# Kernel optimization log

Measured on AMD Instinct MI355X. Metric: run time of the kernel, lower is better.

Reference implementation:

```python
import jax, jax.numpy as jnp
import numpy as np

N, E = 50000, 400000
IN, HID, HEADS, OUT, EDIM = 128, 16, 8, 128, 32


def _lin(key, fan_in, fan_out, bias=True):
    k1, k2 = jax.random.split(key)
    s = 1.0 / np.sqrt(fan_in)
    W = jax.random.uniform(k1, (fan_in, fan_out), jnp.float32, -s, s)
    if bias:
        b = jax.random.uniform(k2, (fan_out,), jnp.float32, -s, s)
        return W, b
    return W


def setup_inputs() -> dict:
    key = jax.random.key(0)
    ks = jax.random.split(key, 16)
    x = jax.random.normal(ks[0], (N, IN), jnp.float32)
    edge_index = jax.random.randint(ks[1], (2, E), 0, N, jnp.int64)
    edge_feats = jax.random.normal(ks[2], (E, EDIM), jnp.float32)
    H1 = HEADS * HID  # 128
    Wq1, bq1 = _lin(ks[3], IN, H1)
    Wk1, bk1 = _lin(ks[4], IN, H1)
    Wv1, bv1 = _lin(ks[5], IN, H1)
    We1 = _lin(ks[6], EDIM, H1, bias=False)
    Ws1, bs1 = _lin(ks[7], IN, H1)
    Wq2, bq2 = _lin(ks[8], H1, OUT)
    Wk2, bk2 = _lin(ks[9], H1, OUT)
    Wv2, bv2 = _lin(ks[10], H1, OUT)
    We2 = _lin(ks[11], EDIM, OUT, bias=False)
    Ws2, bs2 = _lin(ks[12], H1, OUT)
    return dict(x=x, edge_index=edge_index, edge_feats=edge_feats,
                Wq1=Wq1, bq1=bq1, Wk1=Wk1, bk1=bk1, Wv1=Wv1, bv1=bv1, We1=We1, Ws1=Ws1, bs1=bs1,
                Wq2=Wq2, bq2=bq2, Wk2=Wk2, bk2=bk2, Wv2=Wv2, bv2=bv2, We2=We2, Ws2=Ws2, bs2=bs2)


def transformer_conv(x, src, dst, e, Wq, bq, Wk, bk, Wv, bv, We, Ws, bs, heads, ch, concat):
    # PyG TransformerConv: project at nodes, gather to edges.
    n = x.shape[0]
    q = (x @ Wq + bq).reshape(n, heads, ch)[dst]          # [E,H,C]
    k = (x @ Wk + bk).reshape(n, heads, ch)[src]
    v = (x @ Wv + bv).reshape(n, heads, ch)[src]
    ee = (e @ We).reshape(-1, heads, ch)                   # edge conditioning
    k = k + ee
    v = v + ee
    alpha = (q * k).sum(-1) / jnp.sqrt(jnp.asarray(ch, x.dtype))  # [E,H]
    # per-destination segment softmax
    m = jax.ops.segment_max(alpha, dst, num_segments=n)
    m = jnp.where(jnp.isfinite(m), m, 0.0)
    ea = jnp.exp(alpha - m[dst])
    denom = jax.ops.segment_sum(ea, dst, num_segments=n)
    attn = ea / jnp.maximum(denom[dst], 1e-16)
    out = jax.ops.segment_sum(attn[:, :, None] * v, dst, num_segments=n)  # [N,H,C]
    out = out.reshape(n, heads * ch) if concat else out.mean(axis=1)
    return out + x @ Ws + bs  # root_weight skip


def reference(x, edge_index, edge_feats,
              Wq1, bq1, Wk1, bk1, Wv1, bv1, We1, Ws1, bs1,
              Wq2, bq2, Wk2, bk2, Wv2, bv2, We2, Ws2, bs2):
    src, dst = edge_index[0], edge_index[1]
    h = jax.nn.relu(transformer_conv(x, src, dst, edge_feats,
                                     Wq1, bq1, Wk1, bk1, Wv1, bv1, We1, Ws1, bs1,
                                     HEADS, HID, True))
    # dropout p=0.0 (eval) -> identity
    out = jax.nn.relu(transformer_conv(h, src, dst, edge_feats,
                                       Wq2, bq2, Wk2, bk2, Wv2, bv2, We2, Ws2, bs2,
                                       1, OUT, False))
    return out
```

## Files before the change

### kernel.cpp

```cpp
#include <hip/hip_runtime.h>


using u16 = unsigned short;
using u32 = unsigned int;

#define NODES 50000
#define EDGES 400000
#define NB196 196

typedef __attribute__((ext_vector_type(8))) short bf16x8;
typedef __attribute__((ext_vector_type(4))) float f32x4;

__device__ __forceinline__ float bflo(u32 u) { return __uint_as_float(u << 16); }
__device__ __forceinline__ float bfhi(u32 u) { return __uint_as_float(u & 0xffff0000u); }
__device__ __forceinline__ u16 f2bf(float f) {
    u32 u = __float_as_uint(f);
    u += 0x7fffu + ((u >> 16) & 1u);
    return (u16)(u >> 16);
}
__device__ __forceinline__ u32 pack2(float a, float b) {
    return (u32)f2bf(a) | ((u32)f2bf(b) << 16);
}

template <int CTRL>
__device__ __forceinline__ float dpp_addf(float x) {
    int y = __builtin_amdgcn_update_dpp(0, __float_as_int(x), CTRL, 0xF, 0xF, true);
    return x + __int_as_float(y);
}
template <int GRP>
__device__ __forceinline__ float grp_sum(float p, int lane) {
    p = dpp_addf<0xB1>(p);
    p = dpp_addf<0x4E>(p);
    p = dpp_addf<0x141>(p);
    if (GRP == 64) {
        p = dpp_addf<0x140>(p);
        p += __int_as_float(__builtin_amdgcn_ds_swizzle(__float_as_int(p), 0x401F));
        p += __int_as_float(__builtin_amdgcn_ds_bpermute((lane ^ 32) << 2,
                                                         __float_as_int(p)));
    }
    return p;
}

__global__ __launch_bounds__(256) void fill_sentinel(float* __restrict__ out, int n, float val) {
    int i = blockIdx.x * 256 + threadIdx.x;
    if (i < n) out[i] = val;
}

__global__ __launch_bounds__(64) void detect_fmt(const u32* __restrict__ xw,
                                                 const int* __restrict__ eraw,
                                                 int* __restrict__ flags) {
    int lane = threadIdx.x;
    u32 e = (xw[lane] >> 7) & 0xffu;
    unsigned long long sane = __ballot(e >= 90u && e <= 141u);
    unsigned long long zodd = __ballot(eraw[1 + 2 * lane] == 0);
    if (lane == 0) {
        flags[0] = (sane == ~0ull) ? 0 : 1;
        flags[1] = (zodd == ~0ull) ? 1 : 0;
    }
}

struct TPtrs {
    const void* src[10];
    u16*        dst[10];
    int         K[10];
};

__global__ __launch_bounds__(256) void transpose_w(TPtrs P, const int* __restrict__ fmt) {
    int m = blockIdx.x;
    int f = *fmt;
    int K = P.K[m];
    int quarter = (K * 128) >> 2;
    u16* d = P.dst[m];
    int base = blockIdx.y * quarter;
    const float* sf = (const float*)P.src[m];
    const u16*   sb = (const u16*)P.src[m];
    for (int idx = base + threadIdx.x; idx < base + quarter; idx += 256) {
        int k = idx >> 7, n = idx & 127;
        d[n * K + k] = f ? f2bf(sf[idx]) : sb[idx];
    }
}

__global__ __launch_bounds__(256) void count_deg(const int* __restrict__ raw,
                                                 const int* __restrict__ flags,
                                                 int* __restrict__ deg, int E) {
    int e = blockIdx.x * 256 + threadIdx.x;
    if (e < E) {
        int f = flags[1];
        int d = f ? raw[2 * (E + e)] : raw[E + e];
        if ((unsigned)d < (unsigned)NODES) atomicAdd(&deg[d], 1);
    }
}

__device__ __forceinline__ int block_scan256(int v) {
    __shared__ int ws[4];
    int t = threadIdx.x, lane = t & 63, w = t >> 6;
    int x = v;
#pragma unroll
    for (int off = 1; off < 64; off <<= 1) {
        int y = __shfl_up(x, off, 64);
        if (lane >= off) x += y;
    }
    if (lane == 63) ws[w] = x;
    __syncthreads();
#pragma unroll
    for (int j = 0; j < 3; ++j)
        if (j < w) x += ws[j];
    return x;
}

__global__ __launch_bounds__(256) void scan_a(const int* __restrict__ deg,
                                              int* __restrict__ bsum, int n) {
    int i = blockIdx.x * 256 + threadIdx.x;
    int v = (i < n) ? deg[i] : 0;
    int incl = block_scan256(v);
    if (threadIdx.x == 255) bsum[blockIdx.x] = incl;
}

__global__ __launch_bounds__(256) void scan_b(int* __restrict__ bsum, int nb) {
    int t = threadIdx.x;
    int v = (t < nb) ? bsum[t] : 0;
    int incl = block_scan256(v);
    if (t < nb) bsum[t] = incl - v;
}

__global__ __launch_bounds__(256) void scan_c(const int* __restrict__ deg,
                                              const int* __restrict__ bsum,
                                              int* __restrict__ row_ptr,
                                              int* __restrict__ cursor, int n) {
    int b = blockIdx.x;
    int i = b * 256 + threadIdx.x;
    int v = (i < n) ? deg[i] : 0;
    int incl = block_scan256(v) + bsum[b];
    if (i < n) {
        row_ptr[i + 1] = incl;
        cursor[i] = incl - v;
    }
    if (i == 0) row_ptr[0] = 0;
}

__global__ __launch_bounds__(256) void fill_csr(const int* __restrict__ raw,
                                                const int* __restrict__ flags,
                                                int* __restrict__ cursor,
                                                int2* __restrict__ se, int E) {
    int e = blockIdx.x * 256 + threadIdx.x;
    if (e < E) {
        int f = flags[1];
        int d = f ? raw[2 * (E + e)] : raw[E + e];
        int s = f ? raw[2 * e] : raw[e];
        if ((unsigned)d < (unsigned)NODES && (unsigned)s < (unsigned)NODES) {
            int pos = atomicAdd(&cursor[d], 1);
            if ((unsigned)pos < (unsigned)E) se[pos] = make_int2(s, e);
        }
    }
}

__global__ __launch_bounds__(256) void gemm128(
    const void* __restrict__ A, const int* __restrict__ flags, int a_raw,
    const u16* __restrict__ Wt0, const u16* __restrict__ Wt1,
    const u16* __restrict__ Wt2, const u16* __restrict__ Wt3,
    const void* __restrict__ b0, const void* __restrict__ b1,
    const void* __restrict__ b2, const void* __restrict__ b3,
    u16* __restrict__ O0, u16* __restrict__ O1,
    u16* __restrict__ O2, u16* __restrict__ O3,
    int M) {
    constexpr int K = 128;
    constexpr int PAD = K + 8;
    constexpr int KV = K / 8;
    __shared__ u16 Asl[64 * PAD];
    __shared__ u16 Bsl[128 * PAD];

    int f = flags[0];
    const u16* Wt; const void* bias; u16* O;
    switch (blockIdx.y) {
        case 0: Wt = Wt0; bias = b0; O = O0; break;
        case 1: Wt = Wt1; bias = b1; O = O1; break;
        case 2: Wt = Wt2; bias = b2; O = O2; break;
        default: Wt = Wt3; bias = b3; O = O3; break;
    }
    int m0 = blockIdx.x * 64;

    if (a_raw && f) {
        const float* Af = (const float*)A;
        for (int idx = threadIdx.x; idx < 64 * KV; idx += 256) {
            int r = idx / KV, cv = idx % KV;
            int gr = m0 + r;
            uint4 val = make_uint4(0, 0, 0, 0);
            if (gr < M) {
                const float* p = Af + (size_t)gr * K + cv * 8;
                float4 lo = *reinterpret_cast<const float4*>(p);
                float4 hi = *reinterpret_cast<const float4*>(p + 4);
                val = make_uint4(pack2(lo.x, lo.y), pack2(lo.z, lo.w),
                                 pack2(hi.x, hi.y), pack2(hi.z, hi.w));
            }
            *reinterpret_cast<uint4*>(&Asl[r * PAD + cv * 8]) = val;
        }
    } else {
        const u16* Ab = (const u16*)A;
        for (int idx = threadIdx.x; idx < 64 * KV; idx += 256) {
            int r = idx / KV, cv = idx % KV;
            int gr = m0 + r;
            uint4 val = make_uint4(0, 0, 0, 0);
            if (gr < M) val = *reinterpret_cast<const uint4*>(Ab + (size_t)gr * K + cv * 8);
            *reinterpret_cast<uint4*>(&Asl[r * PAD + cv * 8]) = val;
        }
    }
    for (int idx = threadIdx.x; idx < 128 * KV; idx += 256) {
        int r = idx / KV, cv = idx % KV;
        *reinterpret_cast<uint4*>(&Bsl[r * PAD + cv * 8]) =
            *reinterpret_cast<const uint4*>(Wt + r * K + cv * 8);
    }
    __syncthreads();

    int lane = threadIdx.x & 63, wv = threadIdx.x >> 6;
    int l15 = lane & 15;
    int kq = (lane >> 4) * 8;
    f32x4 acc[8] = {};
#pragma unroll
    for (int k0 = 0; k0 < K; k0 += 32) {
        bf16x8 af = *reinterpret_cast<const bf16x8*>(&Asl[(wv * 16 + l15) * PAD + k0 + kq]);
#pragma unroll
        for (int nt = 0; nt < 8; ++nt) {
            bf16x8 bfv = *reinterpret_cast<const bf16x8*>(&Bsl[(nt * 16 + l15) * PAD + k0 + kq]);
            acc[nt] = __builtin_amdgcn_mfma_f32_16x16x32_bf16(af, bfv, acc[nt], 0, 0, 0);
        }
    }

    int rbase = m0 + wv * 16 + (lane >> 4) * 4;
#pragma unroll
    for (int nt = 0; nt < 8; ++nt) {
        int col = nt * 16 + l15;
        float bb = 0.f;
        if (bias) bb = f ? ((const float*)bias)[col] : bflo((u32)((const u16*)bias)[col]);
#pragma unroll
        for (int r = 0; r < 4; ++r) {
            int m = rbase + r;
            if (m < M) O[(size_t)m * 128 + col] = f2bf(acc[nt][r] + bb);
        }
    }
}

__global__ __launch_bounds__(256) void gemm_ee(
    const int2* __restrict__ se, const void* __restrict__ EF,
    const u16* __restrict__ WtE1 , const u16* __restrict__ WtE2,
    const int* __restrict__ flags,
    u16* __restrict__ EE1, u16* __restrict__ EE2, int Etot) {
    constexpr int PAD = 40;
    __shared__ u16 Asl[64 * PAD];
    __shared__ u16 Bsl[2][128 * PAD];
    int p0 = blockIdx.x * 64;
    int f = flags[0];
    bool dual = (EE2 != nullptr);

    {
        int r = threadIdx.x >> 2, seg = threadIdx.x & 3;
        int p = p0 + r;
        int e = (p < Etot) ? se[p].y : 0;
        uint4 val;
        if (f) {
            const float* src = (const float*)EF + (size_t)e * 32 + seg * 8;
            float4 lo = *reinterpret_cast<const float4*>(src);
            float4 hi = *reinterpret_cast<const float4*>(src + 4);
            val = make_uint4(pack2(lo.x, lo.y), pack2(lo.z, lo.w),
                             pack2(hi.x, hi.y), pack2(hi.z, hi.w));
        } else {
            val = *reinterpret_cast<const uint4*>((const u16*)EF + (size_t)e * 32 + seg * 8);
        }
        *reinterpret_cast<uint4*>(&Asl[r * PAD + seg * 8]) = val;
    }
    for (int idx = threadIdx.x; idx < 128 * 4; idx += 256) {
        int r = idx >> 2, seg = idx & 3;
        *reinterpret_cast<uint4*>(&Bsl[0][r * PAD + seg * 8]) =
            *reinterpret_cast<const uint4*>(WtE1 + r * 32 + seg * 8);
    }
    if (dual) {
        for (int idx = threadIdx.x; idx < 128 * 4; idx += 256) {
            int r = idx >> 2, seg = idx & 3;
            *reinterpret_cast<uint4*>(&Bsl[1][r * PAD + seg * 8]) =
                *reinterpret_cast<const uint4*>(WtE2 + r * 32 + seg * 8);
        }
    }
    __syncthreads();

    int lane = threadIdx.x & 63, wv = threadIdx.x >> 6;
    int l15 = lane & 15;
    int kq = (lane >> 4) * 8;
    int rbase = p0 + wv * 16 + (lane >> 4) * 4;
    bf16x8 af = *reinterpret_cast<const bf16x8*>(&Asl[(wv * 16 + l15) * PAD + kq]);

    {
        f32x4 acc[8] = {};
#pragma unroll
        for (int nt = 0; nt < 8; ++nt) {
            bf16x8 bfv = *reinterpret_cast<const bf16x8*>(&Bsl[0][(nt * 16 + l15) * PAD + kq]);
            acc[nt] = __builtin_amdgcn_mfma_f32_16x16x32_bf16(af, bfv, acc[nt], 0, 0, 0);
        }
#pragma unroll
        for (int nt = 0; nt < 8; ++nt) {
            int col = nt * 16 + l15;
#pragma unroll
            for (int r = 0; r < 4; ++r) {
                int p = rbase + r;
                if (p < Etot) EE1[(size_t)p * 128 + col] = f2bf(acc[nt][r]);
            }
        }
    }
    if (dual) {
        f32x4 acc[8] = {};
#pragma unroll
        for (int nt = 0; nt < 8; ++nt) {
            bf16x8 bfv = *reinterpret_cast<const bf16x8*>(&Bsl[1][(nt * 16 + l15) * PAD + kq]);
            acc[nt] = __builtin_amdgcn_mfma_f32_16x16x32_bf16(af, bfv, acc[nt], 0, 0, 0);
        }
#pragma unroll
        for (int nt = 0; nt < 8; ++nt) {
            int col = nt * 16 + l15;
#pragma unroll
            for (int r = 0; r < 4; ++r) {
                int p = rbase + r;
                if (p < Etot) EE2[(size_t)p * 128 + col] = f2bf(acc[nt][r]);
            }
        }
    }
}

template <int HEADS, int F32OUT, int MAT>
__global__ __launch_bounds__(256) void attn_kernel(
    const int* __restrict__ row_ptr, const int2* __restrict__ se,
    const int* __restrict__ flags,
    const u16* __restrict__ Q, const u16* __restrict__ Kn,
    const u16* __restrict__ Vn, const u16* __restrict__ EE,
    const void* __restrict__ EF, const void* __restrict__ We,
    const u16* __restrict__ SK, void* __restrict__ OUT, int nn) {
    int wv = threadIdx.x >> 6, lane = threadIdx.x & 63;
    int node = blockIdx.x * 4 + wv;
    if (node >= nn) return;
    int c0 = lane * 2;
    int f = flags[0];

    u32 qb = *reinterpret_cast<const u32*>(Q + (size_t)node * 128 + c0);
    float q0 = bflo(qb), q1 = bfhi(qb);

    int beg = row_ptr[node], end = row_ptr[node + 1];
    const float scale = (HEADS == 8) ? 0.25f : 0.08838834764831845f;
    constexpr int GRP = (HEADS == 8) ? 8 : 64;

    float l_run = 0.f, a0 = 0.f, a1 = 0.f;

    auto edge_step = [&](u32 kbv, u32 vbv, u32 ebv) {
        float e0 = bflo(ebv), e1 = bfhi(ebv);
        float k0 = bflo(kbv) + e0, k1 = bfhi(kbv) + e1;
        float p = q0 * k0 + q1 * k1;
        p = grp_sum<GRP>(p, lane);
        float w = __expf(p * scale);
        l_run += w;
        a0 = fmaf(w, bflo(vbv) + e0, a0);
        a1 = fmaf(w, bfhi(vbv) + e1, a1);
    };

    if (MAT) {
        int i = beg;
        for (; i + 8 <= end; i += 8) {
            int sA[8];
#pragma unroll
            for (int j = 0; j < 8; ++j) sA[j] = se[i + j].x;
            u32 kb[8], vb[8], eb[8];
#pragma unroll
            for (int j = 0; j < 8; ++j) {
                kb[j] = *reinterpret_cast<const u32*>(Kn + (size_t)sA[j] * 128 + c0);
                vb[j] = *reinterpret_cast<const u32*>(Vn + (size_t)sA[j] * 128 + c0);
                eb[j] = *reinterpret_cast<const u32*>(EE + (size_t)(i + j) * 128 + c0);
            }
#pragma unroll
            for (int j = 0; j < 8; ++j) edge_step(kb[j], vb[j], eb[j]);
        }
        for (; i < end; ++i) {
            int s = se[i].x;
            u32 kbv = *reinterpret_cast<const u32*>(Kn + (size_t)s * 128 + c0);
            u32 vbv = *reinterpret_cast<const u32*>(Vn + (size_t)s * 128 + c0);
            u32 ebv = *reinterpret_cast<const u32*>(EE + (size_t)i * 128 + c0);
            edge_step(kbv, vbv, ebv);
        }
    } else {
        float wf0[32], wf1[32];
        if (f) {
            const float* Wef = (const float*)We;
#pragma unroll
            for (int d = 0; d < 32; ++d) {
                float2 w2 = *reinterpret_cast<const float2*>(Wef + d * 128 + c0);
                wf0[d] = w2.x; wf1[d] = w2.y;
            }
        } else {
            const u16* Web = (const u16*)We;
#pragma unroll
            for (int d = 0; d < 32; ++d) {
                u32 w = *reinterpret_cast<const u32*>(Web + d * 128 + c0);
                wf0[d] = bflo(w); wf1[d] = bfhi(w);
            }
        }
        for (int i = beg; i < end; ++i) {
            int2 p2 = se[i];
            int s = p2.x, e = p2.y;
            u32 kbv = *reinterpret_cast<const u32*>(Kn + (size_t)s * 128 + c0);
            u32 vbv = *reinterpret_cast<const u32*>(Vn + (size_t)s * 128 + c0);
            float efv[32];
            if (f) {
                const float* eff = (const float*)EF + (size_t)e * 32;
#pragma unroll
                for (int t = 0; t < 8; ++t) {
                    float4 q4 = *reinterpret_cast<const float4*>(eff + t * 4);
                    efv[4 * t] = q4.x; efv[4 * t + 1] = q4.y;
                    efv[4 * t + 2] = q4.z; efv[4 * t + 3] = q4.w;
                }
            } else {
                const uint4* efp = reinterpret_cast<const uint4*>((const u16*)EF + (size_t)e * 32);
                uint4 efa = efp[0], efb2 = efp[1], efc = efp[2], efd = efp[3];
                u32 efw[16] = {efa.x, efa.y, efa.z, efa.w, efb2.x, efb2.y, efb2.z, efb2.w,
                               efc.x, efc.y, efc.z, efc.w, efd.x, efd.y, efd.z, efd.w};
#pragma unroll
                for (int t = 0; t < 16; ++t) {
                    efv[2 * t] = bflo(efw[t]);
                    efv[2 * t + 1] = bfhi(efw[t]);
                }
            }
            float ee0 = 0.f, ee1 = 0.f;
#pragma unroll
            for (int t = 0; t < 32; ++t) {
                ee0 = fmaf(efv[t], wf0[t], ee0);
                ee1 = fmaf(efv[t], wf1[t], ee1);
            }
            float k0 = bflo(kbv) + ee0, k1 = bfhi(kbv) + ee1;
            float p = q0 * k0 + q1 * k1;
            p = grp_sum<GRP>(p, lane);
            float w = __expf(p * scale);
            l_run += w;
            a0 = fmaf(w, bflo(vbv) + ee0, a0);
            a1 = fmaf(w, bfhi(vbv) + ee1, a1);
        }
    }

    float inv = 1.f / fmaxf(l_run, 1e-16f);
    u32 sb = *reinterpret_cast<const u32*>(SK + (size_t)node * 128 + c0);
    float o0 = fmaxf(a0 * inv + bflo(sb), 0.f);
    float o1 = fmaxf(a1 * inv + bfhi(sb), 0.f);
    if (F32OUT) {
        *reinterpret_cast<float2*>((float*)OUT + (size_t)node * 128 + c0) = make_float2(o0, o1);
    } else {
        *reinterpret_cast<u32*>((u16*)OUT + (size_t)node * 128 + c0) = pack2(o0, o1);
    }
}

extern "C" void kernel_launch(void* const* d_in, const int* in_sizes, int n_in,
                              void* d_out, int out_size, void* d_ws, size_t ws_size,
                              hipStream_t stream) {
    const int N = NODES, E = EDGES;
    const void* x  = d_in[0];
    const int*  ei = (const int*)d_in[1];
    const void* ef = d_in[2];
    const void* Wq1 = d_in[3];  const void* bq1 = d_in[4];
    const void* Wk1 = d_in[5];  const void* bk1 = d_in[6];
    const void* Wv1 = d_in[7];  const void* bv1 = d_in[8];
    const void* We1 = d_in[9];
    const void* Ws1 = d_in[10]; const void* bs1 = d_in[11];
    const void* Wq2 = d_in[12]; const void* bq2 = d_in[13];
    const void* Wk2 = d_in[14]; const void* bk2 = d_in[15];
    const void* Wv2 = d_in[16]; const void* bv2 = d_in[17];
    const void* We2 = d_in[18];
    const void* Ws2 = d_in[19]; const void* bs2 = d_in[20];

    char* ws = (char*)d_ws;
    size_t off = 0;
    auto carve = [&](size_t bytes) -> void* {
        void* p = ws + off;
        off += (bytes + 255) & ~(size_t)255;
        return p;
    };

    u16* WtQ1 = (u16*)carve(128 * 128 * 2);
    u16* WtK1 = (u16*)carve(128 * 128 * 2);
    u16* WtV1 = (u16*)carve(128 * 128 * 2);
    u16* WtS1 = (u16*)carve(128 * 128 * 2);
    u16* WtQ2 = (u16*)carve(128 * 128 * 2);
    u16* WtK2 = (u16*)carve(128 * 128 * 2);
    u16* WtV2 = (u16*)carve(128 * 128 * 2);
    u16* WtS2 = (u16*)carve(128 * 128 * 2);
    u16* WtE1 = (u16*)carve(128 * 32 * 2);
    u16* WtE2 = (u16*)carve(128 * 32 * 2);
    int* flags   = (int*)carve(256);
    int* deg     = (int*)carve((size_t)N * 4);
    int* bsum    = (int*)carve((size_t)NB196 * 4);
    int* row_ptr = (int*)carve((size_t)(N + 1) * 4);
    int* cursor  = (int*)carve((size_t)N * 4);
    int2* se     = (int2*)carve((size_t)E * 8);
    u16* q  = (u16*)carve((size_t)N * 128 * 2);
    u16* k  = (u16*)carve((size_t)N * 128 * 2);
    u16* v  = (u16*)carve((size_t)N * 128 * 2);
    u16* sk = (u16*)carve((size_t)N * 128 * 2);
    u16* h  = (u16*)carve((size_t)N * 128 * 2);
    const size_t REQ_BASE = off;
    u16* ee1 = (u16*)carve((size_t)E * 128 * 2);
    const size_t REQ_BIG = off;
    u16* ee2 = (u16*)carve((size_t)E * 128 * 2);
    const size_t REQ_2EE = off;
    const bool DUAL  = (ws_size >= REQ_2EE);
    const bool MATOK = (ws_size >= REQ_BIG);

    if (ws_size < REQ_BASE) {
        hipLaunchKernelGGL(fill_sentinel, dim3((out_size + 255) / 256), dim3(256), 0, stream,
                           (float*)d_out, out_size, 16.0f * (float)(ws_size >> 20));
        return;
    }

    hipLaunchKernelGGL(detect_fmt, dim3(1), dim3(64), 0, stream, (const u32*)x, ei, flags);

    TPtrs tp;
    tp.src[0] = Wq1; tp.dst[0] = WtQ1; tp.K[0] = 128;
    tp.src[1] = Wk1; tp.dst[1] = WtK1; tp.K[1] = 128;
    tp.src[2] = Wv1; tp.dst[2] = WtV1; tp.K[2] = 128;
    tp.src[3] = Ws1; tp.dst[3] = WtS1; tp.K[3] = 128;
    tp.src[4] = Wq2; tp.dst[4] = WtQ2; tp.K[4] = 128;
    tp.src[5] = Wk2; tp.dst[5] = WtK2; tp.K[5] = 128;
    tp.src[6] = Wv2; tp.dst[6] = WtV2; tp.K[6] = 128;
    tp.src[7] = Ws2; tp.dst[7] = WtS2; tp.K[7] = 128;
    tp.src[8] = We1; tp.dst[8] = WtE1; tp.K[8] = 32;
    tp.src[9] = We2; tp.dst[9] = WtE2; tp.K[9] = 32;
    hipLaunchKernelGGL(transpose_w, dim3(10, 4), dim3(256), 0, stream, tp, flags);

    (void)hipMemsetAsync(deg, 0, (size_t)N * 4, stream);
    hipLaunchKernelGGL(count_deg, dim3((E + 255) / 256), dim3(256), 0, stream, ei, flags, deg, E);
    hipLaunchKernelGGL(scan_a, dim3(NB196), dim3(256), 0, stream, deg, bsum, N);
    hipLaunchKernelGGL(scan_b, dim3(1), dim3(256), 0, stream, bsum, NB196);
    hipLaunchKernelGGL(scan_c, dim3(NB196), dim3(256), 0, stream, deg, bsum, row_ptr, cursor, N);
    hipLaunchKernelGGL(fill_csr, dim3((E + 255) / 256), dim3(256), 0, stream, ei, flags, cursor, se, E);

    const int gN = (N + 63) / 64;
    const int gE = E / 64;
    const int gA = (N + 3) / 4;

    if (MATOK) {
        hipLaunchKernelGGL(gemm_ee, dim3(gE), dim3(256), 0, stream,
                           se, ef, WtE1, WtE2, flags,
                           ee1, DUAL ? ee2 : (u16*)nullptr, E);
    }

    hipLaunchKernelGGL(gemm128, dim3(gN, 4), dim3(256), 0, stream,
                       x, flags, 1, WtQ1, WtK1, WtV1, WtS1,
                       bq1, bk1, bv1, bs1, q, k, v, sk, N);
    if (MATOK) {
        hipLaunchKernelGGL((attn_kernel<8, 0, 1>), dim3(gA), dim3(256), 0, stream,
                           row_ptr, se, flags, q, k, v, ee1, ef, We1, sk, (void*)h, N);
    } else {
        hipLaunchKernelGGL((attn_kernel<8, 0, 0>), dim3(gA), dim3(256), 0, stream,
                           row_ptr, se, flags, q, k, v, (const u16*)nullptr, ef, We1, sk, (void*)h, N);
    }

    hipLaunchKernelGGL(gemm128, dim3(gN, 4), dim3(256), 0, stream,
                       h, flags, 0, WtQ2, WtK2, WtV2, WtS2,
                       bq2, bk2, bv2, bs2, q, k, v, sk, N);
    if (MATOK) {
        if (!DUAL) {
            hipLaunchKernelGGL(gemm_ee, dim3(gE), dim3(256), 0, stream,
                               se, ef, WtE2, (const u16*)nullptr, flags,
                               ee1, (u16*)nullptr, E);
        }
        hipLaunchKernelGGL((attn_kernel<1, 1, 1>), dim3(gA), dim3(256), 0, stream,
                           row_ptr, se, flags, q, k, v, DUAL ? ee2 : ee1, ef, We2, sk, d_out, N);
    } else {
        hipLaunchKernelGGL((attn_kernel<1, 1, 0>), dim3(gA), dim3(256), 0, stream,
                           row_ptr, se, flags, q, k, v, (const u16*)nullptr, ef, We2, sk, d_out, N);
    }
}
```

Before: 470.5 us.

## Interleave K and V per node, split CSR arrays, transpose MFMA for row-contiguous stores

K and V projections are now written interleaved into one [N,256] buffer, so the attention kernel fetches both with a single 8-byte gather per source node instead of two 4-byte gathers. The CSR int2 array is split into separate srcs and eids arrays, so attention reads only the source indices. The GEMMs swap MFMA operands so each lane holds four consecutive output columns of one row, allowing packed 8-byte stores instead of scattered 2-byte stores. The K/V path still writes 2-byte strided stores into the interleaved layout, which may cost some GEMM store efficiency.

```diff
diff --git a/kernel.cpp b/kernel.cpp
--- a/kernel.cpp
+++ b/kernel.cpp
@@ -141,7 +141,8 @@
 __global__ __launch_bounds__(256) void fill_csr(const int* __restrict__ raw,
                                                 const int* __restrict__ flags,
                                                 int* __restrict__ cursor,
-                                                int2* __restrict__ se, int E) {
+                                                int* __restrict__ srcs,
+                                                int* __restrict__ eids, int E) {
     int e = blockIdx.x * 256 + threadIdx.x;
     if (e < E) {
         int f = flags[1];
@@ -149,7 +150,7 @@
         int s = f ? raw[2 * e] : raw[e];
         if ((unsigned)d < (unsigned)NODES && (unsigned)s < (unsigned)NODES) {
             int pos = atomicAdd(&cursor[d], 1);
-            if ((unsigned)pos < (unsigned)E) se[pos] = make_int2(s, e);
+            if ((unsigned)pos < (unsigned)E) { srcs[pos] = s; eids[pos] = e; }
         }
     }
 }
@@ -160,8 +161,7 @@
     const u16* __restrict__ Wt2, const u16* __restrict__ Wt3,
     const void* __restrict__ b0, const void* __restrict__ b1,
     const void* __restrict__ b2, const void* __restrict__ b3,
-    u16* __restrict__ O0, u16* __restrict__ O1,
-    u16* __restrict__ O2, u16* __restrict__ O3,
+    u16* __restrict__ Oq, u16* __restrict__ KVo, u16* __restrict__ Osk,
     int M) {
     constexpr int K = 128;
     constexpr int PAD = K + 8;
@@ -170,12 +170,13 @@
     __shared__ u16 Bsl[128 * PAD];
 
     int f = flags[0];
-    const u16* Wt; const void* bias; u16* O;
-    switch (blockIdx.y) {
-        case 0: Wt = Wt0; bias = b0; O = O0; break;
-        case 1: Wt = Wt1; bias = b1; O = O1; break;
-        case 2: Wt = Wt2; bias = b2; O = O2; break;
-        default: Wt = Wt3; bias = b3; O = O3; break;
+    int set = blockIdx.y;
+    const u16* Wt; const void* bias;
+    switch (set) {
+        case 0: Wt = Wt0; bias = b0; break;
+        case 1: Wt = Wt1; bias = b1; break;
+        case 2: Wt = Wt2; bias = b2; break;
+        default: Wt = Wt3; bias = b3; break;
     }
     int m0 = blockIdx.x * 64;
 
@@ -213,34 +214,63 @@
 
     int lane = threadIdx.x & 63, wv = threadIdx.x >> 6;
     int l15 = lane & 15;
-    int kq = (lane >> 4) * 8;
+    int quad = lane >> 4;
+    int kq = quad * 8;
+
+    f32x4 b4[8];
+#pragma unroll
+    for (int nt = 0; nt < 8; ++nt) {
+        int col0 = nt * 16 + quad * 4;
+        if (bias) {
+            if (f) {
+                b4[nt] = *reinterpret_cast<const f32x4*>((const float*)bias + col0);
+            } else {
+                uint2 bu = *reinterpret_cast<const uint2*>((const u16*)bias + col0);
+                b4[nt][0] = bflo(bu.x); b4[nt][1] = bfhi(bu.x);
+                b4[nt][2] = bflo(bu.y); b4[nt][3] = bfhi(bu.y);
+            }
+        } else {
+            b4[nt][0] = b4[nt][1] = b4[nt][2] = b4[nt][3] = 0.f;
+        }
+    }
+
     f32x4 acc[8] = {};
 #pragma unroll
     for (int k0 = 0; k0 < K; k0 += 32) {
-        bf16x8 af = *reinterpret_cast<const bf16x8*>(&Asl[(wv * 16 + l15) * PAD + k0 + kq]);
+        bf16x8 xf = *reinterpret_cast<const bf16x8*>(&Asl[(wv * 16 + l15) * PAD + k0 + kq]);
 #pragma unroll
         for (int nt = 0; nt < 8; ++nt) {
-            bf16x8 bfv = *reinterpret_cast<const bf16x8*>(&Bsl[(nt * 16 + l15) * PAD + k0 + kq]);
-            acc[nt] = __builtin_amdgcn_mfma_f32_16x16x32_bf16(af, bfv, acc[nt], 0, 0, 0);
-        }
-    }
-
-    int rbase = m0 + wv * 16 + (lane >> 4) * 4;
-#pragma unroll
-    for (int nt = 0; nt < 8; ++nt) {
-        int col = nt * 16 + l15;
-        float bb = 0.f;
-        if (bias) bb = f ? ((const float*)bias)[col] : bflo((u32)((const u16*)bias)[col]);
-#pragma unroll
-        for (int r = 0; r < 4; ++r) {
-            int m = rbase + r;
-            if (m < M) O[(size_t)m * 128 + col] = f2bf(acc[nt][r] + bb);
+            bf16x8 wf = *reinterpret_cast<const bf16x8*>(&Bsl[(nt * 16 + l15) * PAD + k0 + kq]);
+            acc[nt] = __builtin_amdgcn_mfma_f32_16x16x32_bf16(wf, xf, acc[nt], 0, 0, 0);
+        }
+    }
+
+    int row = m0 + wv * 16 + l15;
+    if (row < M) {
+        if (set == 0 || set == 3) {
+            u16* Orow = (set == 0 ? Oq : Osk) + (size_t)row * 128;
+#pragma unroll
+            for (int nt = 0; nt < 8; ++nt) {
+                uint2 pk;
+                pk.x = pack2(acc[nt][0] + b4[nt][0], acc[nt][1] + b4[nt][1]);
+                pk.y = pack2(acc[nt][2] + b4[nt][2], acc[nt][3] + b4[nt][3]);
+                *reinterpret_cast<uint2*>(Orow + nt * 16 + quad * 4) = pk;
+            }
+        } else {
+            u16* Orow = KVo + (size_t)row * 256 + (set == 2 ? 1 : 0);
+#pragma unroll
+            for (int nt = 0; nt < 8; ++nt) {
+                int col0 = nt * 16 + quad * 4;
+#pragma unroll
+                for (int r = 0; r < 4; ++r)
+                    Orow[(col0 + r) * 2] = f2bf(acc[nt][r] + b4[nt][r]);
+            }
         }
     }
 }
 
 __global__ __launch_bounds__(256) void gemm_ee(
-    const int2* __restrict__ se, const void* __restrict__ EF,
+    const int* __restrict__ eids, const void* __restrict__ EF,
     const u16* __restrict__ WtE1 , const u16* __restrict__ WtE2,
     const int* __restrict__ flags,
     u16* __restrict__ EE1, u16* __restrict__ EE2, int Etot) {
@@ -254,7 +284,7 @@
     {
         int r = threadIdx.x >> 2, seg = threadIdx.x & 3;
         int p = p0 + r;
-        int e = (p < Etot) ? se[p].y : 0;
+        int e = (p < Etot) ? eids[p] : 0;
         uint4 val;
         if (f) {
             const float* src = (const float*)EF + (size_t)e * 32 + seg * 8;
@@ -283,24 +313,27 @@
 
     int lane = threadIdx.x & 63, wv = threadIdx.x >> 6;
     int l15 = lane & 15;
-    int kq = (lane >> 4) * 8;
-    int rbase = p0 + wv * 16 + (lane >> 4) * 4;
-    bf16x8 af = *reinterpret_cast<const bf16x8*>(&Asl[(wv * 16 + l15) * PAD + kq]);
+    int quad = lane >> 4;
+    int kq = quad * 8;
+    int pos = p0 + wv * 16 + l15;
+    bool ok = pos < Etot;
+    bf16x8 ef8 = *reinterpret_cast<const bf16x8*>(&Asl[(wv * 16 + l15) * PAD + kq]);
 
     {
         f32x4 acc[8] = {};
 #pragma unroll
         for (int nt = 0; nt < 8; ++nt) {
-            bf16x8 bfv = *reinterpret_cast<const bf16x8*>(&Bsl[0][(nt * 16 + l15) * PAD + kq]);
-            acc[nt] = __builtin_amdgcn_mfma_f32_16x16x32_bf16(af, bfv, acc[nt], 0, 0, 0);
-        }
-#pragma unroll
-        for (int nt = 0; nt < 8; ++nt) {
-            int col = nt * 16 + l15;
-#pragma unroll
-            for (int r = 0; r < 4; ++r) {
-                int p = rbase + r;
-                if (p < Etot) EE1[(size_t)p * 128 + col] = f2bf(acc[nt][r]);
+            bf16x8 wf = *reinterpret_cast<const bf16x8*>(&Bsl[0][(nt * 16 + l15) * PAD + kq]);
+            acc[nt] = __builtin_amdgcn_mfma_f32_16x16x32_bf16(wf, ef8, acc[nt], 0, 0, 0);
+        }
+        if (ok) {
+            u16* Orow = EE1 + (size_t)pos * 128;
+#pragma unroll
+            for (int nt = 0; nt < 8; ++nt) {
+                uint2 pk;
+                pk.x = pack2(acc[nt][0], acc[nt][1]);
+                pk.y = pack2(acc[nt][2], acc[nt][3]);
+                *reinterpret_cast<uint2*>(Orow + nt * 16 + quad * 4) = pk;
             }
         }
     }
@@ -308,27 +341,90 @@
         f32x4 acc[8] = {};
 #pragma unroll
         for (int nt = 0; nt < 8; ++nt) {
-            bf16x8 bfv = *reinterpret_cast<const bf16x8*>(&Bsl[1][(nt * 16 + l15) * PAD + kq]);
-            acc[nt] = __builtin_amdgcn_mfma_f32_16x16x32_bf16(af, bfv, acc[nt], 0, 0, 0);
-        }
-#pragma unroll
-        for (int nt = 0; nt < 8; ++nt) {
-            int col = nt * 16 + l15;
-#pragma unroll
-            for (int r = 0; r < 4; ++r) {
-                int p = rbase + r;
-                if (p < Etot) EE2[(size_t)p * 128 + col] = f2bf(acc[nt][r]);
-            }
-        }
-    }
-}
-
-template <int HEADS, int F32OUT, int MAT>
+            bf16x8 wf = *reinterpret_cast<const bf16x8*>(&Bsl[1][(nt * 16 + l15) * PAD + kq]);
+            acc[nt] = __builtin_amdgcn_mfma_f32_16x16x32_bf16(wf, ef8, acc[nt], 0, 0, 0);
+        }
+        if (ok) {
+            u16* Orow = EE2 + (size_t)pos * 128;
+#pragma unroll
+            for (int nt = 0; nt < 8; ++nt) {
+                uint2 pk;
+                pk.x = pack2(acc[nt][0], acc[nt][1]);
+                pk.y = pack2(acc[nt][2], acc[nt][3]);
+                *reinterpret_cast<uint2*>(Orow + nt * 16 + quad * 4) = pk;
+            }
+        }
+    }
+}
+
+template <int HEADS, int F32OUT>
 __global__ __launch_bounds__(256) void attn_kernel(
-    const int* __restrict__ row_ptr, const int2* __restrict__ se,
-    const int* __restrict__ flags,
-    const u16* __restrict__ Q, const u16* __restrict__ Kn,
-    const u16* __restrict__ Vn, const u16* __restrict__ EE,
+    const int* __restrict__ row_ptr, const int* __restrict__ srcs,
+    const u16* __restrict__ Q, const u16* __restrict__ KVn,
+    const u16* __restrict__ EE, const u16* __restrict__ SK,
+    void* __restrict__ OUT, int nn) {
+    int wv = threadIdx.x >> 6, lane = threadIdx.x & 63;
+    int node = blockIdx.x * 4 + wv;
+    if (node >= nn) return;
+    int c0 = lane * 2;
+
+    u32 qb = *reinterpret_cast<const u32*>(Q + (size_t)node * 128 + c0);
+    float q0 = bflo(qb), q1 = bfhi(qb);
+
+    int beg = row_ptr[node], end = row_ptr[node + 1];
+    const float scale = (HEADS == 8) ? 0.25f : 0.08838834764831845f;
+    constexpr int GRP = (HEADS == 8) ? 8 : 64;
+
+    float l_run = 0.f, a0 = 0.f, a1 = 0.f;
+
+    auto edge_step = [&](uint2 kvv, u32 ebv) {
+        float e0 = bflo(ebv), e1 = bfhi(ebv);
+        float k0 = bflo(kvv.x) + e0, k1 = bflo(kvv.y) + e1;
+        float p = q0 * k0 + q1 * k1;
+        p = grp_sum<GRP>(p, lane);
+        float w = __expf(p * scale);
+        l_run += w;
+        a0 = fmaf(w, bfhi(kvv.x) + e0, a0);
+        a1 = fmaf(w, bfhi(kvv.y) + e1, a1);
+    };
+
+    int i = beg;
+    for (; i + 8 <= end; i += 8) {
+        int sA[8];
+#pragma unroll
+        for (int j = 0; j < 8; ++j) sA[j] = srcs[i + j];
+        uint2 kv2[8]; u32 eb[8];
+#pragma unroll
+        for (int j = 0; j < 8; ++j) {
+            kv2[j] = *reinterpret_cast<const uint2*>(KVn + (size_t)sA[j] * 256 + c0 * 2);
+            eb[j] = *reinterpret_cast<const u32*>(EE + (size_t)(i + j) * 128 + c0);
+        }
+#pragma unroll
+        for (int j = 0; j < 8; ++j) edge_step(kv2[j], eb[j]);
+    }
+    for (; i < end; ++i) {
+        int s = srcs[i];
+        uint2 kvv = *reinterpret_cast<const uint2*>(KVn + (size_t)s * 256 + c0 * 2);
+        u32 ebv = *reinterpret_cast<const u32*>(EE + (size_t)i * 128 + c0);
+        edge_step(kvv, ebv);
+    }
+
+    float inv = 1.f / fmaxf(l_run, 1e-16f);
+    u32 sb = *reinterpret_cast<const u32*>(SK + (size_t)node * 128 + c0);
+    float o0 = fmaxf(a0 * inv + bflo(sb), 0.f);
+    float o1 = fmaxf(a1 * inv + bfhi(sb), 0.f);
+    if (F32OUT) {
+        *reinterpret_cast<float2*>((float*)OUT + (size_t)node * 128 + c0) = make_float2(o0, o1);
+    } else {
+        *reinterpret_cast<u32*>((u16*)OUT + (size_t)node * 128 + c0) = pack2(o0, o1);
+    }
+}
+
+template <int HEADS, int F32OUT>
+__global__ __launch_bounds__(256) void attn_fused(
+    const int* __restrict__ row_ptr, const int* __restrict__ srcs,
+    const int* __restrict__ eids, const int* __restrict__ flags,
+    const u16* __restrict__ Q, const u16* __restrict__ KVn,
     const void* __restrict__ EF, const void* __restrict__ We,
     const u16* __restrict__ SK, void* __restrict__ OUT, int nn) {
     int wv = threadIdx.x >> 6, lane = threadIdx.x & 63;
@@ -337,105 +433,66 @@
     int c0 = lane * 2;
     int f = flags[0];
 
+    float wf0[32], wf1[32];
+    if (f) {
+        const float* Wef = (const float*)We;
+#pragma unroll
+        for (int d = 0; d < 32; ++d) {
+            float2 w2 = *reinterpret_cast<const float2*>(Wef + d * 128 + c0);
+            wf0[d] = w2.x; wf1[d] = w2.y;
+        }
+    } else {
+        const u16* Web = (const u16*)We;
+#pragma unroll
+        for (int d = 0; d < 32; ++d) {
+            u32 w = *reinterpret_cast<const u32*>(Web + d * 128 + c0);
+            wf0[d] = bflo(w); wf1[d] = bfhi(w);
+        }
+    }
+
     u32 qb = *reinterpret_cast<const u32*>(Q + (size_t)node * 128 + c0);
     float q0 = bflo(qb), q1 = bfhi(qb);
-
     int beg = row_ptr[node], end = row_ptr[node + 1];
     const float scale = (HEADS == 8) ? 0.25f : 0.08838834764831845f;
     constexpr int GRP = (HEADS == 8) ? 8 : 64;
-
     float l_run = 0.f, a0 = 0.f, a1 = 0.f;
 
-    auto edge_step = [&](u32 kbv, u32 vbv, u32 ebv) {
-        float e0 = bflo(ebv), e1 = bfhi(ebv);
-        float k0 = bflo(kbv) + e0, k1 = bfhi(kbv) + e1;
+    for (int i = beg; i < end; ++i) {
+        int s = srcs[i], e = eids[i];
+        uint2 kvv = *reinterpret_cast<const uint2*>(KVn + (size_t)s * 256 + c0 * 2);
+        float efv[32];
+        if (f) {
+            const float* eff = (const float*)EF + (size_t)e * 32;
+#pragma unroll
+            for (int t = 0; t < 8; ++t) {
+                float4 q4 = *reinterpret_cast<const float4*>(eff + t * 4);
+                efv[4 * t] = q4.x; efv[4 * t + 1] = q4.y;
+                efv[4 * t + 2] = q4.z; efv[4 * t + 3] = q4.w;
+            }
+        } else {
+            const uint4* efp = reinterpret_cast<const uint4*>((const u16*)EF + (size_t)e * 32);
+            uint4 ea = efp[0], eb2 = efp[1], ec = efp[2], ed = efp[3];
+            u32 efw[16] = {ea.x, ea.y, ea.z, ea.w, eb2.x, eb2.y, eb2.z, eb2.w,
+                           ec.x, ec.y, ec.z, ec.w, ed.x, ed.y, ed.z, ed.w};
+#pragma unroll
+            for (int t = 0; t < 16; ++t) {
+                efv[2 * t] = bflo(efw[t]);
+                efv[2 * t + 1] = bfhi(efw[t]);
+            }
+        }
+        float ee0 = 0.f, ee1 = 0.f;
+#pragma unroll
+        for (int t = 0; t < 32; ++t) {
+            ee0 = fmaf(efv[t], wf0[t], ee0);
+            ee1 = fmaf(efv[t], wf1[t], ee1);
+        }
+        float k0 = bflo(kvv.x) + ee0, k1 = bflo(kvv.y) + ee1;
         float p = q0 * k0 + q1 * k1;
         p = grp_sum<GRP>(p, lane);
         float w = __expf(p * scale);
         l_run += w;
-        a0 = fmaf(w, bflo(vbv) + e0, a0);
-        a1 = fmaf(w, bfhi(vbv) + e1, a1);
-    };
-
-    if (MAT) {
-        int i = beg;
-        for (; i + 8 <= end; i += 8) {
-            int sA[8];
-#pragma unroll
-            for (int j = 0; j < 8; ++j) sA[j] = se[i + j].x;
-            u32 kb[8], vb[8], eb[8];
-#pragma unroll
-            for (int j = 0; j < 8; ++j) {
-                kb[j] = *reinterpret_cast<const u32*>(Kn + (size_t)sA[j] * 128 + c0);
-                vb[j] = *reinterpret_cast<const u32*>(Vn + (size_t)sA[j] * 128 + c0);
-                eb[j] = *reinterpret_cast<const u32*>(EE + (size_t)(i + j) * 128 + c0);
-            }
-#pragma unroll
-            for (int j = 0; j < 8; ++j) edge_step(kb[j], vb[j], eb[j]);
-        }
-        for (; i < end; ++i) {
-            int s = se[i].x;
-            u32 kbv = *reinterpret_cast<const u32*>(Kn + (size_t)s * 128 + c0);
-            u32 vbv = *reinterpret_cast<const u32*>(Vn + (size_t)s * 128 + c0);
-            u32 ebv = *reinterpret_cast<const u32*>(EE + (size_t)i * 128 + c0);
-            edge_step(kbv, vbv, ebv);
-        }
-    } else {
-        float wf0[32], wf1[32];
-        if (f) {
-            const float* Wef = (const float*)We;
-#pragma unroll
-            for (int d = 0; d < 32; ++d) {
-                float2 w2 = *reinterpret_cast<const float2*>(Wef + d * 128 + c0);
-                wf0[d] = w2.x; wf1[d] = w2.y;
-            }
-        } else {
-            const u16* Web = (const u16*)We;
-#pragma unroll
-            for (int d = 0; d < 32; ++d) {
-                u32 w = *reinterpret_cast<const u32*>(Web + d * 128 + c0);
-                wf0[d] = bflo(w); wf1[d] = bfhi(w);
-            }
-        }
-        for (int i = beg; i < end; ++i) {
-            int2 p2 = se[i];
-            int s = p2.x, e = p2.y;
-            u32 kbv = *reinterpret_cast<const u32*>(Kn + (size_t)s * 128 + c0);
-            u32 vbv = *reinterpret_cast<const u32*>(Vn + (size_t)s * 128 + c0);
-            float efv[32];
-            if (f) {
-                const float* eff = (const float*)EF + (size_t)e * 32;
-#pragma unroll
-                for (int t = 0; t < 8; ++t) {
-                    float4 q4 = *reinterpret_cast<const float4*>(eff + t * 4);
-                    efv[4 * t] = q4.x; efv[4 * t + 1] = q4.y;
-                    efv[4 * t + 2] = q4.z; efv[4 * t + 3] = q4.w;
-                }
-            } else {
-                const uint4* efp = reinterpret_cast<const uint4*>((const u16*)EF + (size_t)e * 32);
-                uint4 efa = efp[0], efb2 = efp[1], efc = efp[2], efd = efp[3];
-                u32 efw[16] = {efa.x, efa.y, efa.z, efa.w, efb2.x, efb2.y, efb2.z, efb2.w,
-                               efc.x, efc.y, efc.z, efc.w, efd.x, efd.y, efd.z, efd.w};
-#pragma unroll
-                for (int t = 0; t < 16; ++t) {
-                    efv[2 * t] = bflo(efw[t]);
-                    efv[2 * t + 1] = bfhi(efw[t]);
-                }
-            }
-            float ee0 = 0.f, ee1 = 0.f;
-#pragma unroll
-            for (int t = 0; t < 32; ++t) {
-                ee0 = fmaf(efv[t], wf0[t], ee0);
-                ee1 = fmaf(efv[t], wf1[t], ee1);
-            }
-            float k0 = bflo(kbv) + ee0, k1 = bfhi(kbv) + ee1;
-            float p = q0 * k0 + q1 * k1;
-            p = grp_sum<GRP>(p, lane);
-            float w = __expf(p * scale);
-            l_run += w;
-            a0 = fmaf(w, bflo(vbv) + ee0, a0);
-            a1 = fmaf(w, bfhi(vbv) + ee1, a1);
-        }
+        a0 = fmaf(w, bfhi(kvv.x) + ee0, a0);
+        a1 = fmaf(w, bfhi(kvv.y) + ee1, a1);
     }
 
     float inv = 1.f / fmaxf(l_run, 1e-16f);
@@ -490,10 +547,10 @@
     int* bsum    = (int*)carve((size_t)NB196 * 4);
     int* row_ptr = (int*)carve((size_t)(N + 1) * 4);
     int* cursor  = (int*)carve((size_t)N * 4);
-    int2* se     = (int2*)carve((size_t)E * 8);
+    int* srcs    = (int*)carve((size_t)E * 4);
+    int* eids    = (int*)carve((size_t)E * 4);
     u16* q  = (u16*)carve((size_t)N * 128 * 2);
-    u16* k  = (u16*)carve((size_t)N * 128 * 2);
-    u16* v  = (u16*)carve((size_t)N * 128 * 2);
+    u16* kv = (u16*)carve((size_t)N * 256 * 2);
     u16* sk = (u16*)carve((size_t)N * 128 * 2);
     u16* h  = (u16*)carve((size_t)N * 128 * 2);
     const size_t REQ_BASE = off;
@@ -530,7 +587,8 @@
     hipLaunchKernelGGL(scan_a, dim3(NB196), dim3(256), 0, stream, deg, bsum, N);
     hipLaunchKernelGGL(scan_b, dim3(1), dim3(256), 0, stream, bsum, NB196);
     hipLaunchKernelGGL(scan_c, dim3(NB196), dim3(256), 0, stream, deg, bsum, row_ptr, cursor, N);
-    hipLaunchKernelGGL(fill_csr, dim3((E + 255) / 256), dim3(256), 0, stream, ei, flags, cursor, se, E);
+    hipLaunchKernelGGL(fill_csr, dim3((E + 255) / 256), dim3(256), 0, stream, ei, flags, cursor,
+                       srcs, eids, E);
 
     const int gN = (N + 63) / 64;
     const int gE = E / 64;
@@ -538,34 +596,34 @@
 
     if (MATOK) {
         hipLaunchKernelGGL(gemm_ee, dim3(gE), dim3(256), 0, stream,
-                           se, ef, WtE1, WtE2, flags,
+                           eids, ef, WtE1, WtE2, flags,
                            ee1, DUAL ? ee2 : (u16*)nullptr, E);
     }
 
     hipLaunchKernelGGL(gemm128, dim3(gN, 4), dim3(256), 0, stream,
                        x, flags, 1, WtQ1, WtK1, WtV1, WtS1,
-                       bq1, bk1, bv1, bs1, q, k, v, sk, N);
+                       bq1, bk1, bv1, bs1, q, kv, sk, N);
     if (MATOK) {
-        hipLaunchKernelGGL((attn_kernel<8, 0, 1>), dim3(gA), dim3(256), 0, stream,
-                           row_ptr, se, flags, q, k, v, ee1, ef, We1, sk, (void*)h, N);
+        hipLaunchKernelGGL((attn_kernel<8, 0>), dim3(gA), dim3(256), 0, stream,
+                           row_ptr, srcs, q, kv, ee1, sk, (void*)h, N);
     } else {
-        hipLaunchKernelGGL((attn_kernel<8, 0, 0>), dim3(gA), dim3(256), 0, stream,
-                           row_ptr, se, flags, q, k, v, (const u16*)nullptr, ef, We1, sk, (void*)h, N);
+        hipLaunchKernelGGL((attn_fused<8, 0>), dim3(gA), dim3(256), 0, stream,
+                           row_ptr, srcs, eids, flags, q, kv, ef, We1, sk, (void*)h, N);
     }
 
     hipLaunchKernelGGL(gemm128, dim3(gN, 4), dim3(256), 0, stream,
                        h, flags, 0, WtQ2, WtK2, WtV2, WtS2,
-                       bq2, bk2, bv2, bs2, q, k, v, sk, N);
+                       bq2, bk2, bv2, bs2, q, kv, sk, N);
     if (MATOK) {
         if (!DUAL) {
             hipLaunchKernelGGL(gemm_ee, dim3(gE), dim3(256), 0, stream,
-                               se, ef, WtE2, (const u16*)nullptr, flags,
+                               eids, ef, WtE2, (const u16*)nullptr, flags,
                                ee1, (u16*)nullptr, E);
         }
-        hipLaunchKernelGGL((attn_kernel<1, 1, 1>), dim3(gA), dim3(256), 0, stream,
-                           row_ptr, se, flags, q, k, v, DUAL ? ee2 : ee1, ef, We2, sk, d_out, N);
+        hipLaunchKernelGGL((attn_kernel<1, 1>), dim3(gA), dim3(256), 0, stream,
+                           row_ptr, srcs, q, kv, DUAL ? ee2 : ee1, sk, d_out, N);
     } else {
-        hipLaunchKernelGGL((attn_kernel<1, 1, 0>), dim3(gA), dim3(256), 0, stream,
-                           row_ptr, se, flags, q, k, v, (const u16*)nullptr, ef, We2, sk, d_out, N);
-    }
-}
+        hipLaunchKernelGGL((attn_fused<1, 1>), dim3(gA), dim3(256), 0, stream,
+                           row_ptr, srcs, eids, flags, q, kv, ef, We2, sk, d_out, N);
+    }
+}
```

Result: slower. 493.1 us (+4.8%).
